# Performance work log

Hardware: AMD Instinct MI355X
Metric: run time of the kernel (lower is better)

The kernel has to match this reference:

```python
import jax, jax.numpy as jnp
import numpy as np

HID = 256
VOC = 50257
N_E_SH = 2
N_E_SP = 2
N_MB = 4
B, S = 8, 512
LN_EPS = 1e-3  # keras LayerNormalization default epsilon
STD = 0.02


def setup_inputs() -> dict:
    key = jax.random.key(0)
    ks = jax.random.split(key, 10)
    x = jax.random.normal(ks[0], (B, S, HID), dtype=jnp.float32)
    # labels drawn in [1, VOC) so the `labels > 0` mask keeps every token (static shape)
    labels = jax.random.randint(ks[1], (B, S), 1, VOC, dtype=jnp.int32)
    xb = jax.random.randint(ks[2], (B, S), 0, N_MB + 1, dtype=jnp.int32)
    W_sh = jax.random.normal(ks[3], (N_E_SH, HID, HID), dtype=jnp.float32) * STD
    b_sh = jax.random.normal(ks[4], (N_E_SH, HID), dtype=jnp.float32) * STD
    W_sp = jax.random.normal(ks[5], (N_MB * N_E_SP, HID, HID), dtype=jnp.float32) * STD
    b_sp = jax.random.normal(ks[6], (N_MB * N_E_SP, HID), dtype=jnp.float32) * STD
    w_gates = jax.random.normal(ks[7], (N_MB, HID, N_E_SH + N_E_SP), dtype=jnp.float32) * STD
    vocab_bias = jax.random.normal(ks[8], (VOC,), dtype=jnp.float32) * STD
    emb = jax.random.normal(ks[9], (VOC, HID), dtype=jnp.float32) * STD  # tied_to.weights[0]
    ln_gamma = jnp.ones((HID,), dtype=jnp.float32)
    ln_beta = jnp.zeros((HID,), dtype=jnp.float32)
    return {"x": x, "labels": labels, "xb": xb, "W_sh": W_sh, "b_sh": b_sh,
            "W_sp": W_sp, "b_sp": b_sp, "w_gates": w_gates,
            "vocab_bias": vocab_bias, "emb": emb,
            "ln_gamma": ln_gamma, "ln_beta": ln_beta}


def _layernorm(h, gamma, beta):
    mu = jnp.mean(h, axis=-1, keepdims=True)
    var = jnp.mean(jnp.square(h - mu), axis=-1, keepdims=True)
    return gamma * (h - mu) * jax.lax.rsqrt(var + LN_EPS) + beta


def reference(x, labels, xb, W_sh, b_sh, W_sp, b_sp, w_gates, vocab_bias, emb, ln_gamma, ln_beta):
    xf = x.reshape(-1, HID)          # [N, H]
    lf = labels.reshape(-1)          # [N], all > 0 => mask gather is identity
    xbf = xb.reshape(-1)             # [N]

    # shared + branch-specific experts: [e, N, H]
    sh = jnp.einsum('nd,edh->enh', xf, W_sh) + b_sh[:, None, :]
    sp = jnp.einsum('nd,edh->enh', xf, W_sp) + b_sp[:, None, :]
    sp = sp.reshape(N_MB, N_E_SP, -1, HID)                       # [t, e_sp, N, H]
    sh_b = jnp.broadcast_to(sh[None], (N_MB, N_E_SH, sh.shape[1], HID))
    merge = jnp.concatenate([sh_b, sp], axis=1)                  # [t, e, N, H]

    gates = jax.nn.softmax(jnp.einsum('nd,tde->tne', xf, w_gates), axis=-1)  # [t, N, e]
    out = jnp.einsum('tend,tne->tnd', merge, gates)              # [t, N, H]

    outputs = jnp.concatenate([jnp.zeros_like(xf)[None], out], axis=0)  # [t+1, N, H]
    oh = jax.nn.one_hot(xbf, N_MB + 1, dtype=jnp.float32)        # [N, t+1]
    e_out = jnp.einsum('tnd,nt->nd', outputs, oh)                # [N, H]

    e_out = _layernorm(e_out, ln_gamma, ln_beta) + xf

    logits = e_out @ emb.T + vocab_bias                          # [N, VOC]
    logp = jax.nn.log_softmax(logits, axis=-1)
    loss = -jnp.take_along_axis(logp, lf[:, None], axis=-1)[:, 0]  # [N]
    prob = jnp.exp(logp)
    return prob, loss
```

## Files before the change

kernel.cpp:

```cpp
#include <hip/hip_runtime.h>

#define HID 256
#define VOC 50257
#define NTOK 4096
#define NCT3 393
#define CG 8
#define TN 128
#define LN_EPS 1e-3f
#define PROB_ELEMS 205852672

typedef __attribute__((ext_vector_type(8))) short bf16x8;
typedef __attribute__((ext_vector_type(4))) float f32x4;
typedef __attribute__((ext_vector_type(16))) float f32x16;

__device__ inline unsigned short f2bf(float f) {
    unsigned int u = __builtin_bit_cast(unsigned int, f);
    unsigned int r = u + 0x7FFFu + ((u >> 16) & 1u);
    return (unsigned short)(r >> 16);
}
__device__ inline float bf2f(unsigned short b) {
    unsigned int u = ((unsigned int)b) << 16;
    return __builtin_bit_cast(float, u);
}

__global__ __launch_bounds__(256) void prep_kernel(
    const float* __restrict__ emb, const float* __restrict__ Wsh,
    const float* __restrict__ Wsp,
    unsigned short* __restrict__ embbf, unsigned short* __restrict__ Wtbf) {
    __shared__ float t[64][65];
    int tid = threadIdx.x;
    if (blockIdx.x < 160) {
        int bx = blockIdx.x % 40, by = blockIdx.x / 40;
        int gcol0 = bx * 64;
        int k0 = by * 64;
        int e = gcol0 >> 8, h0 = gcol0 & 255;
        const float* Wp = (e < 2) ? (Wsh + e * 65536) : (Wsp + (e - 2) * 65536);
#pragma unroll
        for (int i = 0; i < 16; ++i) {
            int id = tid + i * 256;
            int k = id >> 6, h = id & 63;
            t[k][h] = Wp[(k0 + k) * 256 + h0 + h];
        }
        __syncthreads();
#pragma unroll
        for (int i = 0; i < 4; ++i) {
            int id = tid + i * 256;
            int h = id >> 4, kq = id & 15;
            ushort4 o;
            o.x = f2bf(t[kq * 4 + 0][h]); o.y = f2bf(t[kq * 4 + 1][h]);
            o.z = f2bf(t[kq * 4 + 2][h]); o.w = f2bf(t[kq * 4 + 3][h]);
            *reinterpret_cast<ushort4*>(Wtbf + (size_t)(gcol0 + h) * 256 + k0 + kq * 4) = o;
        }
    } else {
        const int n4 = VOC * HID / 4;
        int i = (blockIdx.x - 160) * 256 + tid;
        int stride = (gridDim.x - 160) * 256;
        for (; i < n4; i += stride) {
            float4 v = reinterpret_cast<const float4*>(emb)[i];
            ushort4 o;
            o.x = f2bf(v.x); o.y = f2bf(v.y); o.z = f2bf(v.z); o.w = f2bf(v.w);
            reinterpret_cast<ushort4*>(embbf)[i] = o;
        }
    }
}

__global__ __launch_bounds__(256) void expert_gemm(
    const float* __restrict__ x,
    const unsigned short* __restrict__ Wtbf,
    const float* __restrict__ bsh, const float* __restrict__ bsp,
    float* __restrict__ cexp) {
    __shared__ unsigned short sA[64 * 256];
    __shared__ unsigned short sB[64 * 256];
    int bid = blockIdx.x;
    int rt = bid & 63;
    int ct = bid >> 6;
    int row0 = rt * 64, col0 = ct * 64;
    int tid = threadIdx.x;

#pragma unroll
    for (int i = 0; i < 8; ++i) {
        int id = tid + i * 256;
        int r = id >> 5, c = id & 31;
        const float* xr = x + (size_t)(row0 + r) * 256 + c * 8;
        float4 v0 = *reinterpret_cast<const float4*>(xr);
        float4 v1 = *reinterpret_cast<const float4*>(xr + 4);
        bf16x8 o;
        o[0] = (short)f2bf(v0.x); o[1] = (short)f2bf(v0.y);
        o[2] = (short)f2bf(v0.z); o[3] = (short)f2bf(v0.w);
        o[4] = (short)f2bf(v1.x); o[5] = (short)f2bf(v1.y);
        o[6] = (short)f2bf(v1.z); o[7] = (short)f2bf(v1.w);
        *reinterpret_cast<bf16x8*>(sA + r * 256 + ((c ^ (r & 7)) * 8)) = o;
    }
#pragma unroll
    for (int i = 0; i < 8; ++i) {
        int id = tid + i * 256;
        int j = id >> 5, c = id & 31;
        bf16x8 v = *reinterpret_cast<const bf16x8*>(Wtbf + (size_t)(col0 + j) * 256 + c * 8);
        *reinterpret_cast<bf16x8*>(sB + j * 256 + ((c ^ (j & 7)) * 8)) = v;
    }
    __syncthreads();

    int lane = tid & 63, wave = tid >> 6;
    int wcol = wave * 16;
    int lrow = lane & 15, g = lane >> 4;
    f32x4 zero4 = {0.f, 0.f, 0.f, 0.f};
    f32x4 acc[4];
#pragma unroll
    for (int mf = 0; mf < 4; ++mf) acc[mf] = zero4;

#pragma unroll
    for (int ks = 0; ks < 8; ++ks) {
        int kc = ks * 4 + g;
        int j = wcol + lrow;
        bf16x8 b = *reinterpret_cast<const bf16x8*>(sB + j * 256 + ((kc ^ (j & 7)) * 8));
        bf16x8 a[4];
#pragma unroll
        for (int mf = 0; mf < 4; ++mf) {
            int r = mf * 16 + lrow;
            a[mf] = *reinterpret_cast<const bf16x8*>(sA + r * 256 + ((kc ^ (r & 7)) * 8));
        }
#pragma unroll
        for (int mf = 0; mf < 4; ++mf)
            acc[mf] = __builtin_amdgcn_mfma_f32_16x16x32_bf16(a[mf], b, acc[mf], 0, 0, 0);
    }

    {
        int col = col0 + wcol + lrow;
        int e = col >> 8, h = col & 255;
        float bias = (e < 2) ? bsh[e * 256 + h] : bsp[(e - 2) * 256 + h];
#pragma unroll
        for (int mf = 0; mf < 4; ++mf)
#pragma unroll
            for (int r = 0; r < 4; ++r) {
                int row = row0 + mf * 16 + g * 4 + r;
                cexp[(size_t)row * 2560 + col] = acc[mf][r] + bias;
            }
    }
}

__global__ __launch_bounds__(256) void combine_ln(
    const float* __restrict__ x, const int* __restrict__ xb,
    const float* __restrict__ wg, const float* __restrict__ cexp,
    const float* __restrict__ gamma, const float* __restrict__ beta,
    unsigned short* __restrict__ ebf) {
    __shared__ float sx[256];
    __shared__ float sg[4];
    __shared__ float rs[4], rq[4];
    int n = blockIdx.x, h = threadIdx.x;
    float xv = x[n * 256 + h];
    sx[h] = xv;
    __syncthreads();
    int xbn = xb[n];
    float eo;
    if (xbn == 0) {
        eo = beta[h] + xv;
    } else {
        int t = xbn - 1;
        int wv = h >> 6, lane = h & 63;
        float p = 0.f;
        const float* wgt = wg + t * 1024;
#pragma unroll
        for (int i = 0; i < 4; ++i) {
            int d = lane * 4 + i;
            p += sx[d] * wgt[d * 4 + wv];
        }
#pragma unroll
        for (int off = 32; off; off >>= 1) p += __shfl_down(p, off);
        if (lane == 0) sg[wv] = p;
        __syncthreads();
        float g0 = sg[0], g1 = sg[1], g2 = sg[2], g3 = sg[3];
        float mx = fmaxf(fmaxf(g0, g1), fmaxf(g2, g3));
        float e0 = __expf(g0 - mx), e1 = __expf(g1 - mx);
        float e2 = __expf(g2 - mx), e3 = __expf(g3 - mx);
        float inv = 1.f / (e0 + e1 + e2 + e3);
        const float* cr = cexp + (size_t)n * 2560;
        float o = (e0 * cr[h] + e1 * cr[256 + h] +
                   e2 * cr[512 + t * 512 + h] + e3 * cr[768 + t * 512 + h]) * inv;
        float s = o, q = o * o;
#pragma unroll
        for (int off = 32; off; off >>= 1) { s += __shfl_down(s, off); q += __shfl_down(q, off); }
        if (lane == 0) { rs[wv] = s; rq[wv] = q; }
        __syncthreads();
        float mu = (rs[0] + rs[1] + rs[2] + rs[3]) * (1.f / 256.f);
        float ex2 = (rq[0] + rq[1] + rq[2] + rq[3]) * (1.f / 256.f);
        float var = ex2 - mu * mu;
        eo = gamma[h] * (o - mu) * rsqrtf(var + LN_EPS) + beta[h] + xv;
    }
    ebf[n * 256 + h] = f2bf(eo);
}

template <int PASS>
__global__ __launch_bounds__(512, 2) void big_gemm(
    const unsigned short* __restrict__ ebf,
    const unsigned short* __restrict__ embbf,
    const float* __restrict__ vbias,
    float* __restrict__ psum,
    const float* __restrict__ denom,
    float* __restrict__ prob) {
    __shared__ unsigned short sB[2][TN * 256];

    int bid = blockIdx.x;
    int rt = bid >> 3;
    int cg = bid & 7;
    int row0 = rt * 128;
    int tid = threadIdx.x;
    int wave = tid >> 6, lane = tid & 63;
    int l31 = lane & 31, hi = lane >> 5;
    int wr = wave >> 2, wc = wave & 3;
    int tstart = (cg * NCT3) / CG;
    int tend = ((cg + 1) * NCT3) / CG;
    int nmy = tend - tstart;

    bf16x8 a[2][16];
    {
        const unsigned short* ab =
            ebf + (size_t)(row0 + wr * 64 + l31) * 256 + hi * 8;
#pragma unroll
        for (int mf = 0; mf < 2; ++mf)
#pragma unroll
            for (int ks = 0; ks < 16; ++ks)
                a[mf][ks] = *reinterpret_cast<const bf16x8*>(ab + mf * 32 * 256 + ks * 16);
    }

    auto stage = [&](int ct, int buf) {
        int col0 = ct * TN;
#pragma unroll
        for (int i = 0; i < 8; ++i) {
            int col = i * 16 + wave * 2 + hi;
            int gcol = col0 + col; if (gcol >= VOC) gcol = VOC - 1;
            const unsigned short* src =
                embbf + (size_t)gcol * 256 + ((l31 ^ (col & 7)) * 8);
            unsigned short* dst = (unsigned short*)sB[buf] + (size_t)(i * 512 + wave * 64) * 8;
            __builtin_amdgcn_global_load_lds(
                (const __attribute__((address_space(1))) void*)src,
                (__attribute__((address_space(3))) void*)dst, 16, 0, 0);
        }
    };

    stage(tstart, 0);
    asm volatile("s_waitcnt vmcnt(0)" ::: "memory");
    __syncthreads();

    float invd[2][16];
    if (PASS == 1) {
#pragma unroll
        for (int mf = 0; mf < 2; ++mf)
#pragma unroll
            for (int r = 0; r < 16; ++r) {
                int row = row0 + wr * 64 + mf * 32 + (r & 3) + 8 * (r >> 2) + 4 * hi;
                invd[mf][r] = 1.f / denom[row];
            }
    }
    float es[2][16];
    if (PASS == 0) {
#pragma unroll
        for (int mf = 0; mf < 2; ++mf)
#pragma unroll
            for (int r = 0; r < 16; ++r) es[mf][r] = 0.f;
    }

    f32x16 zz = {0.f,0.f,0.f,0.f,0.f,0.f,0.f,0.f,0.f,0.f,0.f,0.f,0.f,0.f,0.f,0.f};

    for (int it = 0; it < nmy; ++it) {
        int ct = tstart + it;
        if (it + 1 < nmy) stage(ct + 1, (it + 1) & 1);

        int gc = ct * TN + wc * 32 + l31;
        float bvb;
        if (PASS == 0) bvb = (gc < VOC) ? vbias[gc] : -1e4f;
        else           bvb = vbias[(gc < VOC) ? gc : (VOC - 1)];

        const unsigned short* sBc = (const unsigned short*)sB[it & 1];
        int bcol = wc * 32 + l31;
        f32x16 c0 = zz, c1 = zz;
#pragma unroll
        for (int ks = 0; ks < 16; ++ks) {
            int kc = ks * 2 + hi;
            bf16x8 b = *reinterpret_cast<const bf16x8*>(
                sBc + bcol * 256 + ((kc ^ (bcol & 7)) * 8));
            c0 = __builtin_amdgcn_mfma_f32_32x32x16_bf16(a[0][ks], b, c0, 0, 0, 0);
            c1 = __builtin_amdgcn_mfma_f32_32x32x16_bf16(a[1][ks], b, c1, 0, 0, 0);
        }

        asm volatile("s_waitcnt vmcnt(0)" ::: "memory");
        __syncthreads();

        if (PASS == 0) {
#pragma unroll
            for (int r = 0; r < 16; ++r) {
                es[0][r] += __expf(c0[r] + bvb);
                es[1][r] += __expf(c1[r] + bvb);
            }
        } else {
            if (gc < VOC) {
#pragma unroll
                for (int r = 0; r < 16; ++r) {
                    int rowr = row0 + wr * 64 + (r & 3) + 8 * (r >> 2) + 4 * hi;
                    prob[(size_t)rowr * VOC + gc] = __expf(c0[r] + bvb) * invd[0][r];
                    prob[(size_t)(rowr + 32) * VOC + gc] = __expf(c1[r] + bvb) * invd[1][r];
                }
            }
        }
    }

    if (PASS == 0) {
#pragma unroll
        for (int mf = 0; mf < 2; ++mf)
#pragma unroll
            for (int r = 0; r < 16; ++r) {
                float v = es[mf][r];
#pragma unroll
                for (int off = 1; off < 32; off <<= 1) v += __shfl_xor(v, off);
                if (l31 == 0) {
                    int row = row0 + wr * 64 + mf * 32 + (r & 3) + 8 * (r >> 2) + 4 * hi;
                    psum[(size_t)row * 32 + cg * 4 + wc] = v;
                }
            }
    }
}

__global__ __launch_bounds__(64) void finalize_k(
    const float* __restrict__ psum,
    const unsigned short* __restrict__ ebf, const unsigned short* __restrict__ embbf,
    const float* __restrict__ vbias, const int* __restrict__ labels,
    float* __restrict__ denom, float* __restrict__ loss) {
    int n = blockIdx.x, lane = threadIdx.x;
    float s = (lane < 32) ? psum[(size_t)n * 32 + lane] : 0.f;
#pragma unroll
    for (int off = 1; off < 32; off <<= 1) s += __shfl_xor(s, off);
    int lf = labels[n];
    const unsigned short* ev = ebf + n * 256;
    const unsigned short* mv = embbf + (size_t)lf * 256;
    float p = 0.f;
#pragma unroll
    for (int i = 0; i < 4; ++i) p += bf2f(ev[lane * 4 + i]) * bf2f(mv[lane * 4 + i]);
#pragma unroll
    for (int off = 1; off < 64; off <<= 1) p += __shfl_xor(p, off);
    if (lane == 0) {
        denom[n] = s;
        loss[n] = logf(s) - (p + vbias[lf]);
    }
}

extern "C" void kernel_launch(void* const* d_in, const int* in_sizes, int n_in,
                              void* d_out, int out_size, void* d_ws, size_t ws_size,
                              hipStream_t stream) {
    const float* x      = (const float*)d_in[0];
    const int*   labels = (const int*)d_in[1];
    const int*   xb     = (const int*)d_in[2];
    const float* Wsh    = (const float*)d_in[3];
    const float* bsh    = (const float*)d_in[4];
    const float* Wsp    = (const float*)d_in[5];
    const float* bsp    = (const float*)d_in[6];
    const float* wg     = (const float*)d_in[7];
    const float* vbias  = (const float*)d_in[8];
    const float* emb    = (const float*)d_in[9];
    const float* gamma  = (const float*)d_in[10];
    const float* beta   = (const float*)d_in[11];

    char* ws = (char*)d_ws;
    unsigned short* embbf = (unsigned short*)(ws + 2097152);
    unsigned short* Wtbf  = (unsigned short*)(ws + 27828736);
    float* cexp           = (float*)(ws + 29360128);
    unsigned short* ebf   = (unsigned short*)(ws + 71303168);
    float* psum           = (float*)(ws + 73400320);
    float* denom          = (float*)(ws + 73924608);

    float* prob = (float*)d_out;
    float* loss = prob + PROB_ELEMS;

    prep_kernel<<<dim3(2208), dim3(256), 0, stream>>>(emb, Wsh, Wsp, embbf, Wtbf);
    expert_gemm<<<dim3(64 * 40), dim3(256), 0, stream>>>(x, Wtbf, bsh, bsp, cexp);
    combine_ln<<<dim3(NTOK), dim3(256), 0, stream>>>(x, xb, wg, cexp, gamma, beta, ebf);
    big_gemm<0><<<dim3(256), dim3(512), 0, stream>>>(ebf, embbf, vbias, psum, nullptr, nullptr);
    finalize_k<<<dim3(NTOK), dim3(64), 0, stream>>>(psum, ebf, embbf, vbias, labels, denom, loss);
    big_gemm<1><<<dim3(256), dim3(512), 0, stream>>>(ebf, embbf, vbias, nullptr, denom, prob);
}
```

Baseline: 525.5 us.

## Shrink vocab GEMM tiles to 64x64 with 16x16x32 MFMA and double grid

Restructures both passes of the tied-embedding logits GEMM to use 64-row by 64-column tiles, with 16x16x32 bf16 MFMA instead of 32x32x16, and launches twice as many blocks. LDS use per block is halved and fewer registers are held for accumulators and A fragments, so launch bounds now allow 4 blocks per CU. The goal is more parallelism and better latency hiding across the 256 CUs. In exchange, each embedding column tile is reused across half as many rows, which doubles traffic from L2/MALL for the embedding table. Probability stores also become narrower, with 16 contiguous columns per row instead of 32, which could hurt write coalescing.

Result: slower. 554.3 us (+5.5%).

```diff
diff --git a/kernel.cpp b/kernel.cpp
--- a/kernel.cpp
+++ b/kernel.cpp
@@ -3,15 +3,14 @@
 #define HID 256
 #define VOC 50257
 #define NTOK 4096
-#define NCT3 393
+#define NCT64 786
 #define CG 8
-#define TN 128
+#define TN 64
 #define LN_EPS 1e-3f
 #define PROB_ELEMS 205852672
 
 typedef __attribute__((ext_vector_type(8))) short bf16x8;
 typedef __attribute__((ext_vector_type(4))) float f32x4;
-typedef __attribute__((ext_vector_type(16))) float f32x16;
 
 __device__ inline unsigned short f2bf(float f) {
     unsigned int u = __builtin_bit_cast(unsigned int, f);
@@ -190,7 +189,7 @@
 }
 
 template <int PASS>
-__global__ __launch_bounds__(512, 2) void big_gemm(
+__global__ __launch_bounds__(512, 4) void big_gemm(
     const unsigned short* __restrict__ ebf,
     const unsigned short* __restrict__ embbf,
     const float* __restrict__ vbias,
@@ -202,31 +201,32 @@
     int bid = blockIdx.x;
     int rt = bid >> 3;
     int cg = bid & 7;
-    int row0 = rt * 128;
+    int row0 = rt * 64;
     int tid = threadIdx.x;
     int wave = tid >> 6, lane = tid & 63;
-    int l31 = lane & 31, hi = lane >> 5;
+    int l31 = lane & 31;
+    int l15 = lane & 15, kg = lane >> 4;
     int wr = wave >> 2, wc = wave & 3;
-    int tstart = (cg * NCT3) / CG;
-    int tend = ((cg + 1) * NCT3) / CG;
+    int tstart = (cg * NCT64) / CG;
+    int tend = ((cg + 1) * NCT64) / CG;
     int nmy = tend - tstart;
 
-    bf16x8 a[2][16];
+    bf16x8 a[2][8];
     {
         const unsigned short* ab =
-            ebf + (size_t)(row0 + wr * 64 + l31) * 256 + hi * 8;
+            ebf + (size_t)(row0 + wr * 32 + l15) * 256 + kg * 8;
 #pragma unroll
         for (int mf = 0; mf < 2; ++mf)
 #pragma unroll
-            for (int ks = 0; ks < 16; ++ks)
-                a[mf][ks] = *reinterpret_cast<const bf16x8*>(ab + mf * 32 * 256 + ks * 16);
+            for (int ks = 0; ks < 8; ++ks)
+                a[mf][ks] = *reinterpret_cast<const bf16x8*>(ab + mf * 16 * 256 + ks * 32);
     }
 
     auto stage = [&](int ct, int buf) {
         int col0 = ct * TN;
 #pragma unroll
-        for (int i = 0; i < 8; ++i) {
-            int col = i * 16 + wave * 2 + hi;
+        for (int i = 0; i < 4; ++i) {
+            int col = i * 16 + wave * 2 + (lane >> 5);
             int gcol = col0 + col; if (gcol >= VOC) gcol = VOC - 1;
             const unsigned short* src =
                 embbf + (size_t)gcol * 256 + ((l31 ^ (col & 7)) * 8);
@@ -241,45 +241,42 @@
     asm volatile("s_waitcnt vmcnt(0)" ::: "memory");
     __syncthreads();
 
-    float invd[2][16];
+    float invd[2][4];
     if (PASS == 1) {
 #pragma unroll
         for (int mf = 0; mf < 2; ++mf)
 #pragma unroll
-            for (int r = 0; r < 16; ++r) {
-                int row = row0 + wr * 64 + mf * 32 + (r & 3) + 8 * (r >> 2) + 4 * hi;
-                invd[mf][r] = 1.f / denom[row];
-            }
-    }
-    float es[2][16];
+            for (int r = 0; r < 4; ++r)
+                invd[mf][r] = 1.f / denom[row0 + wr * 32 + mf * 16 + kg * 4 + r];
+    }
+    float es[2][4];
     if (PASS == 0) {
 #pragma unroll
         for (int mf = 0; mf < 2; ++mf)
 #pragma unroll
-            for (int r = 0; r < 16; ++r) es[mf][r] = 0.f;
-    }
-
-    f32x16 zz = {0.f,0.f,0.f,0.f,0.f,0.f,0.f,0.f,0.f,0.f,0.f,0.f,0.f,0.f,0.f,0.f};
+            for (int r = 0; r < 4; ++r) es[mf][r] = 0.f;
+    }
+
+    f32x4 zero4 = {0.f, 0.f, 0.f, 0.f};
 
     for (int it = 0; it < nmy; ++it) {
         int ct = tstart + it;
         if (it + 1 < nmy) stage(ct + 1, (it + 1) & 1);
 
-        int gc = ct * TN + wc * 32 + l31;
-        float bvb;
-        if (PASS == 0) bvb = (gc < VOC) ? vbias[gc] : -1e4f;
-        else           bvb = vbias[(gc < VOC) ? gc : (VOC - 1)];
+        int gc = ct * TN + wc * 16 + l15;
+        float bvb = (gc < VOC) ? vbias[gc] : -1e4f;
 
         const unsigned short* sBc = (const unsigned short*)sB[it & 1];
-        int bcol = wc * 32 + l31;
-        f32x16 c0 = zz, c1 = zz;
-#pragma unroll
-        for (int ks = 0; ks < 16; ++ks) {
-            int kc = ks * 2 + hi;
+        int bcol = wc * 16 + l15;
+        f32x4 acc[2];
+        acc[0] = zero4; acc[1] = zero4;
+#pragma unroll
+        for (int ks = 0; ks < 8; ++ks) {
+            int kc = ks * 4 + kg;
             bf16x8 b = *reinterpret_cast<const bf16x8*>(
                 sBc + bcol * 256 + ((kc ^ (bcol & 7)) * 8));
-            c0 = __builtin_amdgcn_mfma_f32_32x32x16_bf16(a[0][ks], b, c0, 0, 0, 0);
-            c1 = __builtin_amdgcn_mfma_f32_32x32x16_bf16(a[1][ks], b, c1, 0, 0, 0);
+            acc[0] = __builtin_amdgcn_mfma_f32_16x16x32_bf16(a[0][ks], b, acc[0], 0, 0, 0);
+            acc[1] = __builtin_amdgcn_mfma_f32_16x16x32_bf16(a[1][ks], b, acc[1], 0, 0, 0);
         }
 
         asm volatile("s_waitcnt vmcnt(0)" ::: "memory");
@@ -287,18 +284,20 @@
 
         if (PASS == 0) {
 #pragma unroll
-            for (int r = 0; r < 16; ++r) {
-                es[0][r] += __expf(c0[r] + bvb);
-                es[1][r] += __expf(c1[r] + bvb);
-            }
+            for (int mf = 0; mf < 2; ++mf)
+#pragma unroll
+                for (int r = 0; r < 4; ++r)
+                    es[mf][r] += __expf(acc[mf][r] + bvb);
         } else {
             if (gc < VOC) {
 #pragma unroll
-                for (int r = 0; r < 16; ++r) {
-                    int rowr = row0 + wr * 64 + (r & 3) + 8 * (r >> 2) + 4 * hi;
-                    prob[(size_t)rowr * VOC + gc] = __expf(c0[r] + bvb) * invd[0][r];
-                    prob[(size_t)(rowr + 32) * VOC + gc] = __expf(c1[r] + bvb) * invd[1][r];
-                }
+                for (int mf = 0; mf < 2; ++mf)
+#pragma unroll
+                    for (int r = 0; r < 4; ++r) {
+                        int row = row0 + wr * 32 + mf * 16 + kg * 4 + r;
+                        prob[(size_t)row * VOC + gc] =
+                            __expf(acc[mf][r] + bvb) * invd[mf][r];
+                    }
             }
         }
     }
@@ -307,12 +306,12 @@
 #pragma unroll
         for (int mf = 0; mf < 2; ++mf)
 #pragma unroll
-            for (int r = 0; r < 16; ++r) {
+            for (int r = 0; r < 4; ++r) {
                 float v = es[mf][r];
 #pragma unroll
-                for (int off = 1; off < 32; off <<= 1) v += __shfl_xor(v, off);
-                if (l31 == 0) {
-                    int row = row0 + wr * 64 + mf * 32 + (r & 3) + 8 * (r >> 2) + 4 * hi;
+                for (int off = 1; off < 16; off <<= 1) v += __shfl_xor(v, off);
+                if (l15 == 0) {
+                    int row = row0 + wr * 32 + mf * 16 + kg * 4 + r;
                     psum[(size_t)row * 32 + cg * 4 + wc] = v;
                 }
             }
@@ -372,7 +371,7 @@
     prep_kernel<<<dim3(2208), dim3(256), 0, stream>>>(emb, Wsh, Wsp, embbf, Wtbf);
     expert_gemm<<<dim3(64 * 40), dim3(256), 0, stream>>>(x, Wtbf, bsh, bsp, cexp);
     combine_ln<<<dim3(NTOK), dim3(256), 0, stream>>>(x, xb, wg, cexp, gamma, beta, ebf);
-    big_gemm<0><<<dim3(256), dim3(512), 0, stream>>>(ebf, embbf, vbias, psum, nullptr, nullptr);
+    big_gemm<0><<<dim3(512), dim3(512), 0, stream>>>(ebf, embbf, vbias, psum, nullptr, nullptr);
     finalize_k<<<dim3(NTOK), dim3(64), 0, stream>>>(psum, ebf, embbf, vbias, labels, denom, loss);
-    big_gemm<1><<<dim3(256), dim3(512), 0, stream>>>(ebf, embbf, vbias, nullptr, denom, prob);
-}
+    big_gemm<1><<<dim3(512), dim3(512), 0, stream>>>(ebf, embbf, vbias, nullptr, denom, prob);
+}
```

## Stage prob tile through swizzled LDS for coalesced float4 global stores

Applied to the files above, without the earlier changes.

In the second pass, the exp-normalized probabilities are first written into the now-free B shared-memory buffer using an XOR-swizzled layout. Each thread then reads one row quarter back and writes it to global memory with aligned float4 stores. Scalar head and tail stores handle rows whose start is not 16-byte aligned, since VOC is odd. This replaces the strided per-lane scalar writes from the MFMA fragment layout, aiming at the dominant prob-write bandwidth cost, and adds an extra barrier per iteration plus LDS traffic.

New measurement: 833.1 us. 1.59x slower.

```diff
diff --git a/kernel.cpp b/kernel.cpp
--- a/kernel.cpp
+++ b/kernel.cpp
@@ -263,12 +263,11 @@
 
     for (int it = 0; it < nmy; ++it) {
         int ct = tstart + it;
+        if (PASS == 1 && it > 0) __syncthreads();
         if (it + 1 < nmy) stage(ct + 1, (it + 1) & 1);
 
         int gc = ct * TN + wc * 32 + l31;
-        float bvb;
-        if (PASS == 0) bvb = (gc < VOC) ? vbias[gc] : -1e4f;
-        else           bvb = vbias[(gc < VOC) ? gc : (VOC - 1)];
+        float bvb = (gc < VOC) ? vbias[gc] : -1e4f;
 
         const unsigned short* sBc = (const unsigned short*)sB[it & 1];
         int bcol = wc * 32 + l31;
@@ -292,12 +291,57 @@
                 es[1][r] += __expf(c1[r] + bvb);
             }
         } else {
-            if (gc < VOC) {
-#pragma unroll
-                for (int r = 0; r < 16; ++r) {
-                    int rowr = row0 + wr * 64 + (r & 3) + 8 * (r >> 2) + 4 * hi;
-                    prob[(size_t)rowr * VOC + gc] = __expf(c0[r] + bvb) * invd[0][r];
-                    prob[(size_t)(rowr + 32) * VOC + gc] = __expf(c1[r] + bvb) * invd[1][r];
+            float* ftile = (float*)sB[it & 1];
+            int cw = wc * 32 + l31;
+            int cwh = cw >> 2, cwl = cw & 3;
+#pragma unroll
+            for (int r = 0; r < 16; ++r) {
+                int rl = wr * 64 + (r & 3) + 8 * (r >> 2) + 4 * hi;
+                ftile[rl * 128 + ((cwh ^ (rl & 31)) << 2) + cwl] =
+                    __expf(c0[r] + bvb) * invd[0][r];
+                int rl2 = rl + 32;
+                ftile[rl2 * 128 + ((cwh ^ (rl2 & 31)) << 2) + cwl] =
+                    __expf(c1[r] + bvb) * invd[1][r];
+            }
+            __syncthreads();
+            int rl = tid >> 2;
+            int q = tid & 3;
+            int row_g = row0 + rl;
+            int C0 = ct * TN;
+            float* pr = prob + (size_t)row_g * VOC;
+            int rx = rl & 31;
+            int o = (-row_g) & 3;
+            int cq = q * 32;
+            for (int c = cq; c < cq + o; ++c) {
+                int gcol = C0 + c;
+                if (gcol < VOC)
+                    pr[gcol] = ftile[rl * 128 + ((((c >> 2) ^ rx)) << 2) + (c & 3)];
+            }
+            int nf4 = (o == 0) ? 8 : 7;
+#pragma unroll
+            for (int k = 0; k < 8; ++k) {
+                if (k >= nf4) break;
+                int c = cq + o + k * 4;
+                int gcol = C0 + c;
+                float4 v;
+                v.x = ftile[rl * 128 + (((((c + 0) >> 2) ^ rx)) << 2) + ((c + 0) & 3)];
+                v.y = ftile[rl * 128 + (((((c + 1) >> 2) ^ rx)) << 2) + ((c + 1) & 3)];
+                v.z = ftile[rl * 128 + (((((c + 2) >> 2) ^ rx)) << 2) + ((c + 2) & 3)];
+                v.w = ftile[rl * 128 + (((((c + 3) >> 2) ^ rx)) << 2) + ((c + 3) & 3)];
+                if (gcol + 3 < VOC) {
+                    *reinterpret_cast<float4*>(pr + gcol) = v;
+                } else {
+                    if (gcol + 0 < VOC) pr[gcol + 0] = v.x;
+                    if (gcol + 1 < VOC) pr[gcol + 1] = v.y;
+                    if (gcol + 2 < VOC) pr[gcol + 2] = v.z;
+                    if (gcol + 3 < VOC) pr[gcol + 3] = v.w;
+                }
+            }
+            if (o > 0) {
+                for (int c = cq + o + 28; c < cq + 32; ++c) {
+                    int gcol = C0 + c;
+                    if (gcol < VOC)
+                        pr[gcol] = ftile[rl * 128 + ((((c >> 2) ^ rx)) << 2) + (c & 3)];
                 }
             }
         }
```
